# Kernel optimization log

Measured on AMD Instinct MI355X. Metric: run time of the kernel, lower is better.

Reference implementation:

```python
import jax, jax.numpy as jnp
import numpy as np

N_NODES = 50000
N_EDGES = 600000
IN_DIM = 128
HID = 128
OUT_DIM = 2
N_GRAPHS = 64
EPS = 1e-12  # F.normalize default eps


def setup_inputs() -> dict:
    key = jax.random.key(0)
    ks = jax.random.split(key, 16)
    s = 0.05
    x = jax.random.normal(ks[0], (N_NODES, IN_DIM), jnp.float32)
    edge_index = jax.random.randint(ks[1], (2, N_EDGES), 0, N_NODES, dtype=jnp.int32)
    batch = jnp.sort(jax.random.randint(ks[2], (N_NODES,), 0, N_GRAPHS, dtype=jnp.int32))
    # GraphSage layer 0: lin (IN->HID), agg_lin (IN+HID -> HID)
    lin_w0 = jax.random.normal(ks[3], (IN_DIM, HID), jnp.float32) * s
    lin_b0 = jnp.zeros((HID,), jnp.float32)
    agg_w0 = jax.random.normal(ks[4], (HID + IN_DIM, HID), jnp.float32) * s
    agg_b0 = jnp.zeros((HID,), jnp.float32)
    # GraphSage layer 1: lin (HID->HID), agg_lin (2*HID -> HID)
    lin_w1 = jax.random.normal(ks[5], (HID, HID), jnp.float32) * s
    lin_b1 = jnp.zeros((HID,), jnp.float32)
    agg_w1 = jax.random.normal(ks[6], (2 * HID, HID), jnp.float32) * s
    agg_b1 = jnp.zeros((HID,), jnp.float32)
    # post_mp: Linear(HID,HID) -> Dropout -> Linear(HID,OUT)
    mp_w1 = jax.random.normal(ks[7], (HID, HID), jnp.float32) * s
    mp_b1 = jnp.zeros((HID,), jnp.float32)
    mp_w2 = jax.random.normal(ks[8], (HID, OUT_DIM), jnp.float32) * s
    mp_b2 = jnp.zeros((OUT_DIM,), jnp.float32)
    return dict(x=x, edge_index=edge_index, batch=batch,
                lin_w0=lin_w0, lin_b0=lin_b0, agg_w0=agg_w0, agg_b0=agg_b0,
                lin_w1=lin_w1, lin_b1=lin_b1, agg_w1=agg_w1, agg_b1=agg_b1,
                mp_w1=mp_w1, mp_b1=mp_b1, mp_w2=mp_w2, mp_b2=mp_b2)


def sage_layer(x, lin_w, lin_b, agg_w, agg_b, src, dst, num_nodes):
    # message: ReLU(Linear(x_j)) gathered along source nodes  [E, HID]
    msg = jax.nn.relu(x[src] @ lin_w + lin_b)
    # aggr='mean' scatter to target nodes
    summed = jax.ops.segment_sum(msg, dst, num_segments=num_nodes)
    deg = jax.ops.segment_sum(jnp.ones((src.shape[0], 1), x.dtype), dst,
                              num_segments=num_nodes)
    agg = summed / jnp.maximum(deg, 1.0)
    # update: ReLU(Linear([aggr, x])) then L2-normalize rows
    h = jax.nn.relu(jnp.concatenate([agg, x], axis=-1) @ agg_w + agg_b)
    norm = jnp.sqrt(jnp.sum(h * h, axis=1, keepdims=True))
    return h / jnp.maximum(norm, EPS)


def reference(x, edge_index, batch,
              lin_w0, lin_b0, agg_w0, agg_b0,
              lin_w1, lin_b1, agg_w1, agg_b1,
              mp_w1, mp_b1, mp_w2, mp_b2):
    src, dst = edge_index[0], edge_index[1]
    n = x.shape[0]
    h = sage_layer(x, lin_w0, lin_b0, agg_w0, agg_b0, src, dst, n)
    # F.relu is a no-op on the non-negative normalized output; dropout p=0 -> identity
    h = sage_layer(h, lin_w1, lin_b1, agg_w1, agg_b1, src, dst, n)
    # global max pool over graphs
    pooled = jax.ops.segment_max(h, batch, num_segments=N_GRAPHS)
    pooled = jnp.where(jnp.isfinite(pooled), pooled, 0.0)  # guard empty graphs
    # post_mp: Linear -> Dropout(identity) -> Linear
    z = (pooled @ mp_w1 + mp_b1) @ mp_w2 + mp_b2
    return jax.nn.log_softmax(z, axis=1)
```

## Files before the change

kernel.cpp:

```cpp
#include <hip/hip_runtime.h>

__device__ __forceinline__ float bf2f(ushort u) {
    union { uint i; float f; } c; c.i = ((uint)u) << 16; return c.f;
}
__device__ __forceinline__ float bf2lo(uint v) {
    union { uint i; float f; } c; c.i = v << 16; return c.f;
}
__device__ __forceinline__ float bf2hi(uint v) {
    union { uint i; float f; } c; c.i = v & 0xffff0000u; return c.f;
}
__device__ __forceinline__ ushort f2bf(float f) {
    union { float f; uint i; } c; c.f = f;
    uint b = c.i;
    uint r = (b + 0x7fffu + ((b >> 16) & 1u)) >> 16;
    return (ushort)r;
}

typedef __bf16 v8bf __attribute__((ext_vector_type(8)));
typedef float  v4f  __attribute__((ext_vector_type(4)));

__global__ __launch_bounds__(256) void sniff_kernel(const uint* __restrict__ words, int* __restrict__ flag) {
    __shared__ int s[256];
    int t = threadIdx.x;
    int bad = 0;
    for (int i = t; i < 2048; i += 256) {
        uint w = words[i];
        uint exp = (w >> 7) & 0xffu;
        if (exp >= 143u) bad++;
    }
    s[t] = bad;
    __syncthreads();
    for (int o = 128; o; o >>= 1) {
        if (t < o) s[t] += s[t + o];
        __syncthreads();
    }
    if (t == 0) *flag = (s[0] > 64) ? 1 : 0;
}

__device__ __forceinline__ ushort load_conv(const void* src, int i, int isf32) {
    return isf32 ? f2bf(((const float*)src)[i]) : ((const ushort*)src)[i];
}

struct SmallSrcs { const void* p[8]; };
__global__ __launch_bounds__(256) void phaseA(
    const void* __restrict__ x, ushort* __restrict__ xb, int nx, int nbconv,
    const void* __restrict__ w0, const void* __restrict__ wa0,
    const void* __restrict__ w1, const void* __restrict__ wa1,
    ushort* __restrict__ t0, ushort* __restrict__ ta0,
    ushort* __restrict__ t1, ushort* __restrict__ ta1,
    SmallSrcs s, ushort* __restrict__ smalldst,
    int* __restrict__ deg, int* __restrict__ pooled, int N, int G,
    const int* __restrict__ flag) {
    int b = blockIdx.x, t = threadIdx.x;
    if (b < nbconv) {
        int idx = b * 256 + t;
        int base = idx * 8;
        if (base + 8 <= nx) {
            if (*flag) {
                const float4* s4 = (const float4*)x;
                float4 a = s4[idx * 2], bb = s4[idx * 2 + 1];
                union { ushort u[8]; uint4 v; } o;
                o.u[0] = f2bf(a.x); o.u[1] = f2bf(a.y); o.u[2] = f2bf(a.z); o.u[3] = f2bf(a.w);
                o.u[4] = f2bf(bb.x); o.u[5] = f2bf(bb.y); o.u[6] = f2bf(bb.z); o.u[7] = f2bf(bb.w);
                *(uint4*)(xb + base) = o.v;
            } else {
                *(uint4*)(xb + base) = ((const uint4*)x)[idx];
            }
        } else {
            int isf = *flag;
            for (int i = base; i < nx; i++) xb[i] = load_conv(x, i, isf);
        }
    } else if (b < nbconv + 452) {
        int idx = (b - nbconv) * 256 + t;
        if (idx < 98304) {
            const void* W; ushort* T; int K; int local;
            if (idx < 16384)      { W = w0;  T = t0;  K = 128; local = idx; }
            else if (idx < 49152) { W = wa0; T = ta0; K = 256; local = idx - 16384; }
            else if (idx < 65536) { W = w1;  T = t1;  K = 128; local = idx - 49152; }
            else                  { W = wa1; T = ta1; K = 256; local = idx - 65536; }
            ushort v = load_conv(W, local, *flag);
            int k = local >> 7;
            int n = local & 127;
            T[(size_t)n * K + k] = v;
        } else {
            int si = idx - 98304;
            if (si < 17282) {
                const int offs[9] = {0, 128, 256, 384, 512, 16896, 17024, 17280, 17282};
                int seg = 0;
                while (si >= offs[seg + 1]) seg++;
                smalldst[si] = load_conv(s.p[seg], si - offs[seg], *flag);
            }
        }
    } else {
        int idx = (b - nbconv - 452) * 256 + t;
        int nd4 = N >> 2;
        int4 z = {0, 0, 0, 0};
        if (idx < nd4) ((int4*)deg)[idx] = z;
        else if (idx == nd4) { for (int i = nd4 * 4; i < N; i++) deg[i] = 0; }
        else if (idx - nd4 - 1 < G * 32) ((int4*)pooled)[idx - nd4 - 1] = z;
    }
}

__global__ __launch_bounds__(256) void count_deg(const int* __restrict__ dst, int* __restrict__ deg, int E) {
    int i = blockIdx.x * 256 + threadIdx.x;
    if (i < E) atomicAdd(&deg[dst[i]], 1);
}

#define SCAN_CHUNK 1024

__global__ __launch_bounds__(256) void chunk_sum_kernel(const int* __restrict__ deg,
                                                        int* __restrict__ csums, int n) {
    __shared__ int s[256];
    int t = threadIdx.x;
    int base = blockIdx.x * SCAN_CHUNK + t * 4;
    int v = 0;
    if (base + 4 <= n) {
        int4 q = *(const int4*)(deg + base);
        v = q.x + q.y + q.z + q.w;
    } else {
        for (int i = base; i < n; i++) v += deg[i];
    }
    s[t] = v;
    __syncthreads();
    for (int o = 128; o; o >>= 1) {
        if (t < o) s[t] += s[t + o];
        __syncthreads();
    }
    if (t == 0) csums[blockIdx.x] = s[0];
}

__global__ __launch_bounds__(256) void scan_phase2(const int* __restrict__ deg,
                                                   const int* __restrict__ csums,
                                                   int* __restrict__ rowptr, int* __restrict__ cursor,
                                                   int n) {
    __shared__ int red[256];
    int t = threadIdx.x, b = blockIdx.x;
    int v = 0;
    for (int i = t; i < b; i += 256) v += csums[i];
    red[t] = v;
    __syncthreads();
    for (int o = 128; o; o >>= 1) {
        if (t < o) red[t] += red[t + o];
        __syncthreads();
    }
    int chunkOff = red[0];
    __syncthreads();
    int base = b * SCAN_CHUNK + t * 4;
    int d0 = 0, d1 = 0, d2 = 0, d3 = 0;
    if (base + 4 <= n) {
        int4 q = *(const int4*)(deg + base);
        d0 = q.x; d1 = q.y; d2 = q.z; d3 = q.w;
    } else {
        if (base < n)     d0 = deg[base];
        if (base + 1 < n) d1 = deg[base + 1];
        if (base + 2 < n) d2 = deg[base + 2];
        if (base + 3 < n) d3 = deg[base + 3];
    }
    int s4 = d0 + d1 + d2 + d3;
    red[t] = s4;
    __syncthreads();
    for (int o = 1; o < 256; o <<= 1) {
        int u = (t >= o) ? red[t - o] : 0;
        __syncthreads();
        red[t] += u;
        __syncthreads();
    }
    int run = chunkOff + red[t] - s4;
    if (base < n)     { rowptr[base]     = run; cursor[base]     = run; run += d0; }
    if (base + 1 < n) { rowptr[base + 1] = run; cursor[base + 1] = run; run += d1; }
    if (base + 2 < n) { rowptr[base + 2] = run; cursor[base + 2] = run; run += d2; }
    if (base + 3 < n) { rowptr[base + 3] = run; cursor[base + 3] = run; run += d3; }
    if (n >= base && n < base + 4) rowptr[n] = run;
}

__global__ __launch_bounds__(256) void fill_kernel(const int* __restrict__ src, const int* __restrict__ dst,
                                                   int* __restrict__ cursor, int* __restrict__ csr_src, int E) {
    int i = blockIdx.x * 256 + threadIdx.x;
    if (i < E) {
        int pos = atomicAdd(&cursor[dst[i]], 1);
        csr_src[pos] = src[i];
    }
}

template <int NSTAGE, bool NORM, bool POOL, bool FUSE>
__global__ __launch_bounds__(256) void gemm_kernel(
    const ushort* __restrict__ A0, const ushort* __restrict__ A1,
    const ushort* __restrict__ Bt, const ushort* __restrict__ bias,
    ushort* __restrict__ Cout, int M,
    const int* __restrict__ batchv, int* __restrict__ pooled,
    const ushort* __restrict__ Bt2, const ushort* __restrict__ bias2,
    ushort* __restrict__ Mout) {
    constexpr int LDSN = FUSE ? (128 * 136 + 128 * 72) : (2 * 128 * 72);
    __shared__ __bf16 lds[LDSN];
    __shared__ int PoolLoc[POOL ? 8 * 128 : 1];
    __bf16* As = lds;
    __bf16* Bs = lds + 128 * 72;
    const int t = threadIdx.x;
    const int w = t >> 6, lane = t & 63, ln = lane & 15, q = lane >> 4;
    const int blockRow = blockIdx.x * 128;
    const int K = NSTAGE * 128;

    if (POOL) {
        for (int i = t; i < 8 * 128; i += 256) PoolLoc[i] = 0;
    }

    v4f acc[2][8];
#pragma unroll
    for (int i = 0; i < 2; i++)
#pragma unroll
        for (int j = 0; j < 8; j++) acc[i][j] = (v4f){0.f, 0.f, 0.f, 0.f};

    for (int kc = 0; kc < K; kc += 64) {
        const ushort* Ap = (kc < 128) ? A0 : A1;
        int kin = kc & 127;
#pragma unroll
        for (int i = 0; i < 4; i++) {
            int c = i * 256 + t;
            int row = c >> 3, c8 = c & 7;
            int grow = blockRow + row; if (grow >= M) grow = M - 1;
            *(uint4*)&As[row * 72 + c8 * 8] = *(const uint4*)(Ap + (size_t)grow * 128 + kin + c8 * 8);
            *(uint4*)&Bs[row * 72 + c8 * 8] = *(const uint4*)(Bt + (size_t)row * K + kc + c8 * 8);
        }
        __syncthreads();
#pragma unroll
        for (int k0 = 0; k0 < 64; k0 += 32) {
            v8bf a0 = *(const v8bf*)&As[(w * 32 + ln) * 72 + k0 + q * 8];
            v8bf a1 = *(const v8bf*)&As[(w * 32 + 16 + ln) * 72 + k0 + q * 8];
#pragma unroll
            for (int nt = 0; nt < 8; nt++) {
                v8bf b = *(const v8bf*)&Bs[(nt * 16 + ln) * 72 + k0 + q * 8];
                acc[0][nt] = __builtin_amdgcn_mfma_f32_16x16x32_bf16(a0, b, acc[0][nt], 0, 0, 0);
                acc[1][nt] = __builtin_amdgcn_mfma_f32_16x16x32_bf16(a1, b, acc[1][nt], 0, 0, 0);
            }
        }
        __syncthreads();
    }

    float biasf[8];
#pragma unroll
    for (int nt = 0; nt < 8; nt++) biasf[nt] = bf2f(bias[nt * 16 + ln]);

    const int minB = POOL ? batchv[blockRow < M ? blockRow : M - 1] : 0;
    __bf16* Hs = lds;
    ushort* HsU = (ushort*)Hs;

#pragma unroll
    for (int mt = 0; mt < 2; mt++) {
        float v[8][4];
#pragma unroll
        for (int nt = 0; nt < 8; nt++)
#pragma unroll
            for (int r = 0; r < 4; r++) {
                float x = acc[mt][nt][r] + biasf[nt];
                v[nt][r] = x > 0.f ? x : 0.f;
            }
        float inv[4];
        if (NORM) {
#pragma unroll
            for (int r = 0; r < 4; r++) {
                float p = 0.f;
#pragma unroll
                for (int nt = 0; nt < 8; nt++) p += v[nt][r] * v[nt][r];
                p += __shfl_xor(p, 1);
                p += __shfl_xor(p, 2);
                p += __shfl_xor(p, 4);
                p += __shfl_xor(p, 8);
                inv[r] = 1.0f / fmaxf(sqrtf(p), 1e-12f);
            }
        }
        int rowloc = w * 32 + mt * 16 + q * 4;
#pragma unroll
        for (int r = 0; r < 4; r++) {
            int grow = blockRow + rowloc + r;
            if (POOL) {
                if (grow < M) {
                    int b = batchv[grow];
                    int rel = b - minB;
#pragma unroll
                    for (int nt = 0; nt < 8; nt++) {
                        float x = v[nt][r] * inv[r];
                        int xi = __float_as_int(x);
                        if (rel < 8) atomicMax(&PoolLoc[rel * 128 + nt * 16 + ln], xi);
                        else         atomicMax(&pooled[b * 128 + nt * 16 + ln], xi);
                    }
                }
            } else {
#pragma unroll
                for (int nt = 0; nt < 8; nt++) {
                    float x = NORM ? v[nt][r] * inv[r] : v[nt][r];
                    ushort xb = f2bf(x);
                    if (grow < M) Cout[(size_t)grow * 128 + nt * 16 + ln] = xb;
                    if (FUSE) HsU[(rowloc + r) * 136 + nt * 16 + ln] = xb;
                }
            }
        }
    }

    if (POOL) {
        __syncthreads();
        int lastRow = blockRow + 127; if (lastRow >= M) lastRow = M - 1;
        int span = batchv[lastRow] - minB + 1;
        if (span > 8) span = 8;
        for (int i = t; i < span * 128; i += 256) {
            int vv = PoolLoc[i];
            if (vv != 0) atomicMax(&pooled[(minB + (i >> 7)) * 128 + (i & 127)], vv);
        }
    }

    if (FUSE) {
        __bf16* Bs2 = lds + 128 * 136;
        v4f acc2[2][8];
#pragma unroll
        for (int i = 0; i < 2; i++)
#pragma unroll
            for (int j = 0; j < 8; j++) acc2[i][j] = (v4f){0.f, 0.f, 0.f, 0.f};

        for (int kc = 0; kc < 128; kc += 64) {
#pragma unroll
            for (int i = 0; i < 4; i++) {
                int c = i * 256 + t;
                int row = c >> 3, c8 = c & 7;
                *(uint4*)&Bs2[row * 72 + c8 * 8] = *(const uint4*)(Bt2 + (size_t)row * 128 + kc + c8 * 8);
            }
            __syncthreads();
#pragma unroll
            for (int k0 = 0; k0 < 64; k0 += 32) {
                v8bf a0 = *(const v8bf*)&Hs[(w * 32 + ln) * 136 + kc + k0 + q * 8];
                v8bf a1 = *(const v8bf*)&Hs[(w * 32 + 16 + ln) * 136 + kc + k0 + q * 8];
#pragma unroll
                for (int nt = 0; nt < 8; nt++) {
                    v8bf b = *(const v8bf*)&Bs2[(nt * 16 + ln) * 72 + k0 + q * 8];
                    acc2[0][nt] = __builtin_amdgcn_mfma_f32_16x16x32_bf16(a0, b, acc2[0][nt], 0, 0, 0);
                    acc2[1][nt] = __builtin_amdgcn_mfma_f32_16x16x32_bf16(a1, b, acc2[1][nt], 0, 0, 0);
                }
            }
            __syncthreads();
        }

        float biasf2[8];
#pragma unroll
        for (int nt = 0; nt < 8; nt++) biasf2[nt] = bf2f(bias2[nt * 16 + ln]);
#pragma unroll
        for (int mt = 0; mt < 2; mt++) {
            int rowbase = blockRow + w * 32 + mt * 16 + q * 4;
#pragma unroll
            for (int r = 0; r < 4; r++) {
                int grow = rowbase + r;
                if (grow < M) {
#pragma unroll
                    for (int nt = 0; nt < 8; nt++) {
                        float x = acc2[mt][nt][r] + biasf2[nt];
                        Mout[(size_t)grow * 128 + nt * 16 + ln] = f2bf(x > 0.f ? x : 0.f);
                    }
                }
            }
        }
    }
}

__global__ __launch_bounds__(256) void aggregate_kernel(
    const ushort* __restrict__ msg, const int* __restrict__ rowptr,
    const int* __restrict__ csr_src, ushort* __restrict__ agg, int n) {
    int wid = (int)((blockIdx.x * 256u + threadIdx.x) >> 6);
    int lane = threadIdx.x & 63;
    int sub = lane >> 4;
    int l16 = lane & 15;
    if (wid >= n) return;
    int start = rowptr[wid], end = rowptr[wid + 1];
    float a[8] = {0.f, 0.f, 0.f, 0.f, 0.f, 0.f, 0.f, 0.f};
#pragma unroll 2
    for (int j = start + sub; j < end; j += 4) {
        int s = csr_src[j];
        uint4 v = *(const uint4*)(msg + (size_t)s * 128 + l16 * 8);
        a[0] += bf2lo(v.x); a[1] += bf2hi(v.x);
        a[2] += bf2lo(v.y); a[3] += bf2hi(v.y);
        a[4] += bf2lo(v.z); a[5] += bf2hi(v.z);
        a[6] += bf2lo(v.w); a[7] += bf2hi(v.w);
    }
#pragma unroll
    for (int i = 0; i < 8; i++) {
        a[i] += __shfl_xor(a[i], 16);
        a[i] += __shfl_xor(a[i], 32);
    }
    if (sub == 0) {
        float inv = 1.0f / fmaxf((float)(end - start), 1.0f);
        union { ushort u[8]; uint4 v; } o;
#pragma unroll
        for (int i = 0; i < 8; i++) o.u[i] = f2bf(a[i] * inv);
        *(uint4*)(agg + (size_t)wid * 128 + l16 * 8) = o.v;
    }
}

__global__ __launch_bounds__(256) void final_kernel(const float* __restrict__ pooled,
                                                    const ushort* __restrict__ small,
                                                    void* __restrict__ out, int G,
                                                    const int* __restrict__ flag) {
    __shared__ float P[128];
    __shared__ float Thalf[128];
    __shared__ float T[128];
    __shared__ float R0[128], R1[128];
    const ushort* w1 = small + 512;
    const ushort* b1 = small + 16896;
    const ushort* w2 = small + 17024;
    const ushort* b2 = small + 17280;
    int g = blockIdx.x;
    int t = threadIdx.x;
    int j = t & 127, half = t >> 7;
    if (t < 128) P[t] = pooled[g * 128 + t];
    __syncthreads();
    float acc = 0.f;
    int k0 = half * 64;
#pragma unroll 8
    for (int k = k0; k < k0 + 64; k++) acc += P[k] * bf2f(w1[k * 128 + j]);
    if (half == 0) Thalf[j] = acc;
    __syncthreads();
    if (half == 1) T[j] = Thalf[j] + acc + bf2f(b1[j]);
    __syncthreads();
    if (t < 128) {
        float tv = T[t];
        R0[t] = tv * bf2f(w2[t * 2]);
        R1[t] = tv * bf2f(w2[t * 2 + 1]);
    }
    __syncthreads();
    for (int o = 64; o; o >>= 1) {
        if (t < o) { R0[t] += R0[t + o]; R1[t] += R1[t + o]; }
        __syncthreads();
    }
    if (t == 0) {
        float z0 = R0[0] + bf2f(b2[0]);
        float z1 = R1[0] + bf2f(b2[1]);
        float m = fmaxf(z0, z1);
        float l = m + logf(expf(z0 - m) + expf(z1 - m));
        float o0 = z0 - l, o1 = z1 - l;
        if (*flag) {
            ((float*)out)[2 * g]     = o0;
            ((float*)out)[2 * g + 1] = o1;
        } else {
            ((ushort*)out)[2 * g]     = f2bf(o0);
            ((ushort*)out)[2 * g + 1] = f2bf(o1);
        }
    }
}

extern "C" void kernel_launch(void* const* d_in, const int* in_sizes, int n_in,
                              void* d_out, int out_size, void* d_ws, size_t ws_size,
                              hipStream_t stream) {
    const void* x      = d_in[0];
    const int*  ei     = (const int*)d_in[1];
    const int*  batch  = (const int*)d_in[2];

    const int N = in_sizes[0] / 128;
    const int E = in_sizes[1] / 2;
    const int G = out_size / 2;
    const int* srcIdx = ei;
    const int* dstIdx = ei + E;

    char* ws = (char*)d_ws;
    size_t off = 0;
    auto alloc = [&](size_t bytes) -> void* {
        off = (off + 255) & ~(size_t)255;
        void* p = ws + off;
        off += bytes;
        return p;
    };
    int*    flag    = (int*)alloc(4);
    int*    deg     = (int*)alloc((size_t)N * 4);
    int*    rowptr  = (int*)alloc((size_t)(N + 1) * 4);
    int*    cursor  = (int*)alloc((size_t)N * 4);
    int*    csr_src = (int*)alloc((size_t)E * 4);
    int*    csums   = (int*)alloc(((size_t)N / SCAN_CHUNK + 2) * 4);
    ushort* Wt0     = (ushort*)alloc(128 * 128 * 2);
    ushort* WtA0    = (ushort*)alloc(256 * 128 * 2);
    ushort* Wt1     = (ushort*)alloc(128 * 128 * 2);
    ushort* WtA1    = (ushort*)alloc(256 * 128 * 2);
    ushort* small   = (ushort*)alloc(17282 * 2);
    ushort* xb      = (ushort*)alloc((size_t)N * 128 * 2);
    ushort* msg     = (ushort*)alloc((size_t)N * 128 * 2);
    ushort* agg     = (ushort*)alloc((size_t)N * 128 * 2);
    ushort* h0      = (ushort*)alloc((size_t)N * 128 * 2);
    int*    pooled  = (int*)alloc((size_t)G * 128 * 4);

    sniff_kernel<<<1, 256, 0, stream>>>((const uint*)x, flag);

    SmallSrcs ss;
    ss.p[0] = d_in[4];  ss.p[1] = d_in[6];  ss.p[2] = d_in[8];  ss.p[3] = d_in[10];
    ss.p[4] = d_in[11]; ss.p[5] = d_in[12]; ss.p[6] = d_in[13]; ss.p[7] = d_in[14];
    int nbconv = (N * 128 + 2047) / 2048;
    int nbzero = ((N / 4 + 1 + G * 32) + 255) / 256;
    phaseA<<<nbconv + 452 + nbzero, 256, 0, stream>>>(
        x, xb, N * 128, nbconv,
        d_in[3], d_in[5], d_in[7], d_in[9],
        Wt0, WtA0, Wt1, WtA1, ss, small, deg, pooled, N, G, flag);

    int gb = (N + 127) / 128;
    int ab = (N + 3) / 4;
    int eb = (E + 255) / 256;

    gemm_kernel<1, false, false, false><<<gb, 256, 0, stream>>>(
        xb, xb, Wt0, small + 0, msg, N, nullptr, nullptr, nullptr, nullptr, nullptr);

    count_deg<<<eb, 256, 0, stream>>>(dstIdx, deg, E);
    int nchunks = (N + SCAN_CHUNK - 1) / SCAN_CHUNK;
    chunk_sum_kernel<<<nchunks, 256, 0, stream>>>(deg, csums, N);
    scan_phase2<<<N / SCAN_CHUNK + 1, 256, 0, stream>>>(deg, csums, rowptr, cursor, N);
    fill_kernel<<<eb, 256, 0, stream>>>(srcIdx, dstIdx, cursor, csr_src, E);

    aggregate_kernel<<<ab, 256, 0, stream>>>(msg, rowptr, csr_src, agg, N);
    gemm_kernel<2, true, false, true><<<gb, 256, 0, stream>>>(
        agg, xb, WtA0, small + 128, h0, N, nullptr, nullptr, Wt1, small + 256, msg);

    aggregate_kernel<<<ab, 256, 0, stream>>>(msg, rowptr, csr_src, agg, N);
    gemm_kernel<2, true, true, false><<<gb, 256, 0, stream>>>(
        agg, h0, WtA1, small + 384, nullptr, N, batch, pooled, nullptr, nullptr, nullptr);

    final_kernel<<<G, 256, 0, stream>>>((const float*)pooled, small, d_out, G, flag);
}
```

Before: 273.5 us.

## Fold dtype sniff into phaseA and load full 128-wide K tiles in GEMM

Removes the standalone single-block sniff kernel and has every phaseA block redundantly compute the fp32-vs-bf16 detection from the first 2048 words, saving a launch and a serial dependency. The GEMM kernel now stages an entire 128-wide K slice of A and B into padded 136-stride LDS tiles per stage, not two 64-wide chunks, which halves the barrier count. The fused second GEMM loads its weight in one shot. This raises static LDS use to about 68KB per block, which may reduce occupancy, and every phaseA block now does extra redundant global reads for the sniff.

```diff
diff --git a/kernel.cpp b/kernel.cpp
--- a/kernel.cpp
+++ b/kernel.cpp
@@ -18,24 +18,6 @@
 
 typedef __bf16 v8bf __attribute__((ext_vector_type(8)));
 typedef float  v4f  __attribute__((ext_vector_type(4)));
-
-__global__ __launch_bounds__(256) void sniff_kernel(const uint* __restrict__ words, int* __restrict__ flag) {
-    __shared__ int s[256];
-    int t = threadIdx.x;
-    int bad = 0;
-    for (int i = t; i < 2048; i += 256) {
-        uint w = words[i];
-        uint exp = (w >> 7) & 0xffu;
-        if (exp >= 143u) bad++;
-    }
-    s[t] = bad;
-    __syncthreads();
-    for (int o = 128; o; o >>= 1) {
-        if (t < o) s[t] += s[t + o];
-        __syncthreads();
-    }
-    if (t == 0) *flag = (s[0] > 64) ? 1 : 0;
-}
 
 __device__ __forceinline__ ushort load_conv(const void* src, int i, int isf32) {
     return isf32 ? f2bf(((const float*)src)[i]) : ((const ushort*)src)[i];
@@ -50,13 +32,32 @@
     ushort* __restrict__ t1, ushort* __restrict__ ta1,
     SmallSrcs s, ushort* __restrict__ smalldst,
     int* __restrict__ deg, int* __restrict__ pooled, int N, int G,
-    const int* __restrict__ flag) {
+    int* __restrict__ flagOut) {
+    __shared__ int sred[256];
     int b = blockIdx.x, t = threadIdx.x;
+    {
+        const uint* words = (const uint*)x;
+        int bad = 0;
+        for (int i = t; i < 2048; i += 256) {
+            uint w = words[i];
+            uint exp = (w >> 7) & 0xffu;
+            if (exp >= 143u) bad++;
+        }
+        sred[t] = bad;
+        __syncthreads();
+        for (int o = 128; o; o >>= 1) {
+            if (t < o) sred[t] += sred[t + o];
+            __syncthreads();
+        }
+    }
+    const int isf = sred[0] > 64 ? 1 : 0;
+    if (b == 0 && t == 0) *flagOut = isf;
+
     if (b < nbconv) {
         int idx = b * 256 + t;
         int base = idx * 8;
         if (base + 8 <= nx) {
-            if (*flag) {
+            if (isf) {
                 const float4* s4 = (const float4*)x;
                 float4 a = s4[idx * 2], bb = s4[idx * 2 + 1];
                 union { ushort u[8]; uint4 v; } o;
@@ -67,7 +68,6 @@
                 *(uint4*)(xb + base) = ((const uint4*)x)[idx];
             }
         } else {
-            int isf = *flag;
             for (int i = base; i < nx; i++) xb[i] = load_conv(x, i, isf);
         }
     } else if (b < nbconv + 452) {
@@ -78,7 +78,7 @@
             else if (idx < 49152) { W = wa0; T = ta0; K = 256; local = idx - 16384; }
             else if (idx < 65536) { W = w1;  T = t1;  K = 128; local = idx - 49152; }
             else                  { W = wa1; T = ta1; K = 256; local = idx - 65536; }
-            ushort v = load_conv(W, local, *flag);
+            ushort v = load_conv(W, local, isf);
             int k = local >> 7;
             int n = local & 127;
             T[(size_t)n * K + k] = v;
@@ -88,7 +88,7 @@
                 const int offs[9] = {0, 128, 256, 384, 512, 16896, 17024, 17280, 17282};
                 int seg = 0;
                 while (si >= offs[seg + 1]) seg++;
-                smalldst[si] = load_conv(s.p[seg], si - offs[seg], *flag);
+                smalldst[si] = load_conv(s.p[seg], si - offs[seg], isf);
             }
         }
     } else {
@@ -190,11 +190,9 @@
     const int* __restrict__ batchv, int* __restrict__ pooled,
     const ushort* __restrict__ Bt2, const ushort* __restrict__ bias2,
     ushort* __restrict__ Mout) {
-    constexpr int LDSN = FUSE ? (128 * 136 + 128 * 72) : (2 * 128 * 72);
-    __shared__ __bf16 lds[LDSN];
+    __shared__ __bf16 AsT[128 * 136];
+    __shared__ __bf16 BsT[128 * 136];
     __shared__ int PoolLoc[POOL ? 8 * 128 : 1];
-    __bf16* As = lds;
-    __bf16* Bs = lds + 128 * 72;
     const int t = threadIdx.x;
     const int w = t >> 6, lane = t & 63, ln = lane & 15, q = lane >> 4;
     const int blockRow = blockIdx.x * 128;
@@ -210,25 +208,25 @@
 #pragma unroll
         for (int j = 0; j < 8; j++) acc[i][j] = (v4f){0.f, 0.f, 0.f, 0.f};
 
-    for (int kc = 0; kc < K; kc += 64) {
-        const ushort* Ap = (kc < 128) ? A0 : A1;
-        int kin = kc & 127;
-#pragma unroll
-        for (int i = 0; i < 4; i++) {
+#pragma unroll
+    for (int st = 0; st < NSTAGE; st++) {
+        const ushort* Ap = st ? A1 : A0;
+#pragma unroll
+        for (int i = 0; i < 8; i++) {
             int c = i * 256 + t;
-            int row = c >> 3, c8 = c & 7;
+            int row = c >> 4, k8 = (c & 15) * 8;
             int grow = blockRow + row; if (grow >= M) grow = M - 1;
-            *(uint4*)&As[row * 72 + c8 * 8] = *(const uint4*)(Ap + (size_t)grow * 128 + kin + c8 * 8);
-            *(uint4*)&Bs[row * 72 + c8 * 8] = *(const uint4*)(Bt + (size_t)row * K + kc + c8 * 8);
-        }
-        __syncthreads();
-#pragma unroll
-        for (int k0 = 0; k0 < 64; k0 += 32) {
-            v8bf a0 = *(const v8bf*)&As[(w * 32 + ln) * 72 + k0 + q * 8];
-            v8bf a1 = *(const v8bf*)&As[(w * 32 + 16 + ln) * 72 + k0 + q * 8];
+            *(uint4*)&AsT[row * 136 + k8] = *(const uint4*)(Ap + (size_t)grow * 128 + k8);
+            *(uint4*)&BsT[row * 136 + k8] = *(const uint4*)(Bt + (size_t)row * K + st * 128 + k8);
+        }
+        __syncthreads();
+#pragma unroll
+        for (int k0 = 0; k0 < 128; k0 += 32) {
+            v8bf a0 = *(const v8bf*)&AsT[(w * 32 + ln) * 136 + k0 + q * 8];
+            v8bf a1 = *(const v8bf*)&AsT[(w * 32 + 16 + ln) * 136 + k0 + q * 8];
 #pragma unroll
             for (int nt = 0; nt < 8; nt++) {
-                v8bf b = *(const v8bf*)&Bs[(nt * 16 + ln) * 72 + k0 + q * 8];
+                v8bf b = *(const v8bf*)&BsT[(nt * 16 + ln) * 136 + k0 + q * 8];
                 acc[0][nt] = __builtin_amdgcn_mfma_f32_16x16x32_bf16(a0, b, acc[0][nt], 0, 0, 0);
                 acc[1][nt] = __builtin_amdgcn_mfma_f32_16x16x32_bf16(a1, b, acc[1][nt], 0, 0, 0);
             }
@@ -241,8 +239,7 @@
     for (int nt = 0; nt < 8; nt++) biasf[nt] = bf2f(bias[nt * 16 + ln]);
 
     const int minB = POOL ? batchv[blockRow < M ? blockRow : M - 1] : 0;
-    __bf16* Hs = lds;
-    ushort* HsU = (ushort*)Hs;
+    ushort* HsU = (ushort*)AsT;
 
 #pragma unroll
     for (int mt = 0; mt < 2; mt++) {
@@ -308,33 +305,30 @@
     }
 
     if (FUSE) {
-        __bf16* Bs2 = lds + 128 * 136;
+#pragma unroll
+        for (int i = 0; i < 8; i++) {
+            int c = i * 256 + t;
+            int row = c >> 4, k8 = (c & 15) * 8;
+            *(uint4*)&BsT[row * 136 + k8] = *(const uint4*)(Bt2 + (size_t)row * 128 + k8);
+        }
+        __syncthreads();
+
         v4f acc2[2][8];
 #pragma unroll
         for (int i = 0; i < 2; i++)
 #pragma unroll
             for (int j = 0; j < 8; j++) acc2[i][j] = (v4f){0.f, 0.f, 0.f, 0.f};
 
-        for (int kc = 0; kc < 128; kc += 64) {
-#pragma unroll
-            for (int i = 0; i < 4; i++) {
-                int c = i * 256 + t;
-                int row = c >> 3, c8 = c & 7;
-                *(uint4*)&Bs2[row * 72 + c8 * 8] = *(const uint4*)(Bt2 + (size_t)row * 128 + kc + c8 * 8);
-            }
-            __syncthreads();
-#pragma unroll
-            for (int k0 = 0; k0 < 64; k0 += 32) {
-                v8bf a0 = *(const v8bf*)&Hs[(w * 32 + ln) * 136 + kc + k0 + q * 8];
-                v8bf a1 = *(const v8bf*)&Hs[(w * 32 + 16 + ln) * 136 + kc + k0 + q * 8];
-#pragma unroll
-                for (int nt = 0; nt < 8; nt++) {
-                    v8bf b = *(const v8bf*)&Bs2[(nt * 16 + ln) * 72 + k0 + q * 8];
-                    acc2[0][nt] = __builtin_amdgcn_mfma_f32_16x16x32_bf16(a0, b, acc2[0][nt], 0, 0, 0);
-                    acc2[1][nt] = __builtin_amdgcn_mfma_f32_16x16x32_bf16(a1, b, acc2[1][nt], 0, 0, 0);
-                }
-            }
-            __syncthreads();
+#pragma unroll
+        for (int k0 = 0; k0 < 128; k0 += 32) {
+            v8bf a0 = *(const v8bf*)&AsT[(w * 32 + ln) * 136 + k0 + q * 8];
+            v8bf a1 = *(const v8bf*)&AsT[(w * 32 + 16 + ln) * 136 + k0 + q * 8];
+#pragma unroll
+            for (int nt = 0; nt < 8; nt++) {
+                v8bf b = *(const v8bf*)&BsT[(nt * 16 + ln) * 136 + k0 + q * 8];
+                acc2[0][nt] = __builtin_amdgcn_mfma_f32_16x16x32_bf16(a0, b, acc2[0][nt], 0, 0, 0);
+                acc2[1][nt] = __builtin_amdgcn_mfma_f32_16x16x32_bf16(a1, b, acc2[1][nt], 0, 0, 0);
+            }
         }
 
         float biasf2[8];
@@ -480,8 +474,6 @@
     ushort* h0      = (ushort*)alloc((size_t)N * 128 * 2);
     int*    pooled  = (int*)alloc((size_t)G * 128 * 4);
 
-    sniff_kernel<<<1, 256, 0, stream>>>((const uint*)x, flag);
-
     SmallSrcs ss;
     ss.p[0] = d_in[4];  ss.p[1] = d_in[6];  ss.p[2] = d_in[8];  ss.p[3] = d_in[10];
     ss.p[4] = d_in[11]; ss.p[5] = d_in[12]; ss.p[6] = d_in[13]; ss.p[7] = d_in[14];
```

New measurement: 274.2 us. About the same (+0.3%).
